# Performance work log

Measured on AMD Instinct MI355X. Metric: run time of the kernel, lower is better.

Reference implementation:

```python
import jax, jax.numpy as jnp
import numpy as np

B, S, I, H, O = 4096, 512, 1, 16, 1


def setup_inputs() -> dict:
    key = jax.random.key(0)
    ks = jax.random.split(key, 7)
    bound = 1.0 / np.sqrt(H)
    return {
        "x": jax.random.normal(ks[0], (B, S, I), dtype=jnp.float32),
        "W_ih": jax.random.uniform(ks[1], (H, I), minval=-bound, maxval=bound, dtype=jnp.float32),
        "W_hh": jax.random.uniform(ks[2], (H, H), minval=-bound, maxval=bound, dtype=jnp.float32),
        "b_ih": jax.random.uniform(ks[3], (H,), minval=-bound, maxval=bound, dtype=jnp.float32),
        "b_hh": jax.random.uniform(ks[4], (H,), minval=-bound, maxval=bound, dtype=jnp.float32),
        "W_fc": jax.random.uniform(ks[5], (O, H), minval=-bound, maxval=bound, dtype=jnp.float32),
        "b_fc": jax.random.uniform(ks[6], (O,), minval=-bound, maxval=bound, dtype=jnp.float32),
    }


def reference(x, W_ih, W_hh, b_ih, b_hh, W_fc, b_fc):
    # Vanilla RNN (tanh): h_t = tanh(x_t W_ih^T + b_ih + h_{t-1} W_hh^T + b_hh)
    # Precompute input projections for all timesteps in one GEMM: [B,S,H]
    x_proj = jnp.einsum('bsi,hi->bsh', x, W_ih) + b_ih + b_hh

    def step(h, xp_t):  # h: [B,H], xp_t: [B,H]
        h_new = jnp.tanh(xp_t + h @ W_hh.T)
        return h_new, None

    h0 = jnp.zeros((x.shape[0], W_hh.shape[0]), dtype=x.dtype)
    h_last, _ = jax.lax.scan(step, h0, jnp.swapaxes(x_proj, 0, 1))  # scan over S
    # out[:, -1, :] -> final linear
    return h_last @ W_fc.T + b_fc
```

## Files before the change

kernel.cpp:

```cpp
#include <hip/hip_runtime.h>


#define S2LE 2.8853900817779268f

typedef float float4_ __attribute__((ext_vector_type(4)));

#define ROTI(v, N) __builtin_amdgcn_mov_dpp((v), 0x120 + (N), 0xF, 0xF, 0)
#define ROTF(v, N) __int_as_float(__builtin_amdgcn_mov_dpp(__float_as_int(v), 0x120 + (N), 0xF, 0xF, 0))

__global__ __launch_bounds__(64) void rnn_kernel(
    const float* __restrict__ x,
    const float* __restrict__ W_ih,
    const float* __restrict__ W_hh,
    const float* __restrict__ b_ih,
    const float* __restrict__ b_hh,
    const float* __restrict__ W_fc,
    const float* __restrict__ b_fc,
    float* __restrict__ out)
{
    const int li = (int)(threadIdx.x & 15u);
    const int bs = (int)((threadIdx.x >> 4) & 1u);
    const int q  = (int)((threadIdx.x >> 5) & 1u);
    const int b  = (int)(blockIdx.x * 2u + bs);

    const float* __restrict__ row = W_hh + li * 16;

    float sw = 0.0f;
#pragma unroll
    for (int j = 0; j < 16; ++j) sw += row[j];

    const float wsc = -2.0f * S2LE;

    const int rq = (li + 8 * q) & 15;
    float w0 = wsc * row[rq];
    float w1 = wsc * row[ROTI(rq, 1)];
    float w2 = wsc * row[ROTI(rq, 2)];
    float w3 = wsc * row[ROTI(rq, 3)];
    float w4 = wsc * row[ROTI(rq, 4)];
    float w5 = wsc * row[ROTI(rq, 5)];
    float w6 = wsc * row[ROTI(rq, 6)];
    float w7 = wsc * row[ROTI(rq, 7)];

    const float wih  = W_ih[li] * S2LE * 0.5f;
    const float bias = (b_ih[li] + b_hh[li] + sw) * S2LE * 0.5f;
    const float wfc  = q ? 0.0f : W_fc[li];
    const float bfc  = b_fc[0];

    const float4_* __restrict__ xv = (const float4_*)(x + (size_t)b * 512);

    float g = 0.5f;

#define STEP(XP) do { \
    float a0 = (XP), a1; \
    asm volatile( \
        "s_nop 1\n\t" \
        "v_fmac_f32 %0, %2, %3\n\t" \
        "v_mul_f32_dpp %1, %2, %7  row_ror:4 row_mask:0xf bank_mask:0xf\n\t" \
        "v_fmac_f32_dpp %0, %2, %4 row_ror:1 row_mask:0xf bank_mask:0xf\n\t" \
        "v_fmac_f32_dpp %1, %2, %8 row_ror:5 row_mask:0xf bank_mask:0xf\n\t" \
        "v_fmac_f32_dpp %0, %2, %5 row_ror:2 row_mask:0xf bank_mask:0xf\n\t" \
        "v_fmac_f32_dpp %1, %2, %9 row_ror:6 row_mask:0xf bank_mask:0xf\n\t" \
        "v_fmac_f32_dpp %0, %2, %6 row_ror:3 row_mask:0xf bank_mask:0xf\n\t" \
        "v_fmac_f32_dpp %1, %2, %10 row_ror:7 row_mask:0xf bank_mask:0xf\n\t" \
        "v_add_f32 %0, %0, %1\n\t"                     \
        "v_mov_b32 %1, %0\n\t"                         \
        "s_nop 1\n\t" \
        "v_permlane32_swap_b32 %1, %0\n\t"             \
        "v_add_f32 %0, %0, %1\n\t"                     \
        "s_nop 1\n\t" \
        "v_mov_b32_dpp %0, %0 row_ror:8 row_mask:0xc bank_mask:0xf\n\t" \
        : "+v"(a0), "=&v"(a1) \
        : "v"(g), \
          "v"(w0), "v"(w1), "v"(w2), "v"(w3), \
          "v"(w4), "v"(w5), "v"(w6), "v"(w7)); \
    float e_ = __builtin_amdgcn_exp2f(a0); \
    g = __builtin_amdgcn_rcpf(e_ + 1.0f); \
} while (0)

#define BLOCK(BUF) do { \
    _Pragma("unroll") \
    for (int j = 0; j < 4; ++j) { \
        STEP(fmaf((BUF)[j][0], wih, bias)); \
        STEP(fmaf((BUF)[j][1], wih, bias)); \
        STEP(fmaf((BUF)[j][2], wih, bias)); \
        STEP(fmaf((BUF)[j][3], wih, bias)); \
    } \
} while (0)

    float4_ bufA[4], bufB[4];
#pragma unroll
    for (int j = 0; j < 4; ++j) bufA[j] = xv[j];

#pragma unroll 1
    for (int i = 0; i < 32; i += 2) {
#pragma unroll
        for (int j = 0; j < 4; ++j) bufB[j] = xv[(4 * (i + 1) + j) & 127];
        BLOCK(bufA);
#pragma unroll
        for (int j = 0; j < 4; ++j) bufA[j] = xv[(4 * (i + 2) + j) & 127];
        BLOCK(bufB);
    }
#undef BLOCK
#undef STEP

    float p = fmaf(-2.0f * wfc, g, wfc);
    p += ROTF(p, 8);
    p += ROTF(p, 4);
    p += ROTF(p, 2);
    p += ROTF(p, 1);
    if ((threadIdx.x & 47u) == 0) out[b] = p + bfc;
}

extern "C" void kernel_launch(void* const* d_in, const int* in_sizes, int n_in,
                              void* d_out, int out_size, void* d_ws, size_t ws_size,
                              hipStream_t stream) {
    const float* x    = (const float*)d_in[0];
    const float* W_ih = (const float*)d_in[1];
    const float* W_hh = (const float*)d_in[2];
    const float* b_ih = (const float*)d_in[3];
    const float* b_hh = (const float*)d_in[4];
    const float* W_fc = (const float*)d_in[5];
    const float* b_fc = (const float*)d_in[6];
    float* out = (float*)d_out;

    rnn_kernel<<<2048, 64, 0, stream>>>(x, W_ih, W_hh, b_ih, b_hh, W_fc, b_fc, out);
}
```

Baseline: 106.4 us.

## Compute recurrent matvec with MFMA f16 hi/lo split, sixteen batches per wave

Replaces the DPP-rotation matvec with two chained v_mfma_f32_16x16x16_f16 ops per timestep. W_hh is split into fp16 high and low parts to keep accuracy, and the hidden state is carried in fp16 as the B operand. Each wave now processes 16 batch rows instead of 2, so the grid shrinks from 2048 to 256 blocks. The aim is to amortise the serial recurrence across more batches per instruction. The cost is fewer waves per CU to hide latency, MFMA latency sitting on the critical path, and rounding the hidden state to fp16.

```diff
diff --git a/kernel.cpp b/kernel.cpp
--- a/kernel.cpp
+++ b/kernel.cpp
@@ -3,10 +3,28 @@
 
 #define S2LE 2.8853900817779268f
 
-typedef float float4_ __attribute__((ext_vector_type(4)));
+typedef float    float4_ __attribute__((ext_vector_type(4)));
+typedef _Float16 half4_  __attribute__((ext_vector_type(4)));
 
-#define ROTI(v, N) __builtin_amdgcn_mov_dpp((v), 0x120 + (N), 0xF, 0xF, 0)
-#define ROTF(v, N) __int_as_float(__builtin_amdgcn_mov_dpp(__float_as_int(v), 0x120 + (N), 0xF, 0xF, 0))
+#if defined(__has_builtin)
+#if __has_builtin(__builtin_amdgcn_mfma_f32_16x16x16f16)
+#define HAVE_MFMA_BUILTIN 1
+#endif
+#endif
+
+#ifdef HAVE_MFMA_BUILTIN
+#define MFMA16(A, B, C) __builtin_amdgcn_mfma_f32_16x16x16f16((A), (B), (C), 0, 0, 0)
+#else
+static __device__ __forceinline__ float4_ mfma16_asm(half4_ a, half4_ b, float4_ c) {
+    asm volatile("s_nop 1\n\t"
+                 "v_mfma_f32_16x16x16_f16 %0, %1, %2, %0\n\t"
+                 "s_nop 7\n\t"
+                 "s_nop 7"
+                 : "+v"(c) : "v"(a), "v"(b));
+    return c;
+}
+#define MFMA16(A, B, C) mfma16_asm((A), (B), (C))
+#endif
 
 __global__ __launch_bounds__(64) void rnn_kernel(
     const float* __restrict__ x,
@@ -18,72 +36,69 @@
     const float* __restrict__ b_fc,
     float* __restrict__ out)
 {
-    const int li = (int)(threadIdx.x & 15u);
-    const int bs = (int)((threadIdx.x >> 4) & 1u);
-    const int q  = (int)((threadIdx.x >> 5) & 1u);
-    const int b  = (int)(blockIdx.x * 2u + bs);
-
-    const float* __restrict__ row = W_hh + li * 16;
-
-    float sw = 0.0f;
-#pragma unroll
-    for (int j = 0; j < 16; ++j) sw += row[j];
+    const int l   = (int)threadIdx.x;
+    const int col = l & 15;
+    const int qr  = l >> 4;
+    const int i4  = qr * 4;
+    const int b   = (int)(blockIdx.x * 16u + (unsigned)col);
 
     const float wsc = -2.0f * S2LE;
 
-    const int rq = (li + 8 * q) & 15;
-    float w0 = wsc * row[rq];
-    float w1 = wsc * row[ROTI(rq, 1)];
-    float w2 = wsc * row[ROTI(rq, 2)];
-    float w3 = wsc * row[ROTI(rq, 3)];
-    float w4 = wsc * row[ROTI(rq, 4)];
-    float w5 = wsc * row[ROTI(rq, 5)];
-    float w6 = wsc * row[ROTI(rq, 6)];
-    float w7 = wsc * row[ROTI(rq, 7)];
+    half4_ a_hi, a_lo;
+#pragma unroll
+    for (int r = 0; r < 4; ++r) {
+        float u = wsc * W_hh[col * 16 + i4 + r];
+        _Float16 hi = (_Float16)u;
+        a_hi[r] = hi;
+        a_lo[r] = (_Float16)(u - (float)hi);
+    }
 
-    const float wih  = W_ih[li] * S2LE * 0.5f;
-    const float bias = (b_ih[li] + b_hh[li] + sw) * S2LE * 0.5f;
-    const float wfc  = q ? 0.0f : W_fc[li];
-    const float bfc  = b_fc[0];
+    float wihS[4], biasS[4], wfcr[4];
+#pragma unroll
+    for (int r = 0; r < 4; ++r) {
+        const int ri = i4 + r;
+        float rs = 0.0f;
+#pragma unroll
+        for (int k = 0; k < 16; ++k) rs += W_hh[ri * 16 + k];
+        wihS[r]  = W_ih[ri] * S2LE;
+        biasS[r] = (rs + b_ih[ri] + b_hh[ri]) * S2LE;
+        wfcr[r]  = W_fc[ri];
+    }
+    float cfc = b_fc[0];
+#pragma unroll
+    for (int k = 0; k < 16; ++k) cfc += W_fc[k];
 
     const float4_* __restrict__ xv = (const float4_*)(x + (size_t)b * 512);
 
-    float g = 0.5f;
+    half4_ gB = {(_Float16)0.5f, (_Float16)0.5f, (_Float16)0.5f, (_Float16)0.5f};
+    float4_ gf = {0.5f, 0.5f, 0.5f, 0.5f};
 
-#define STEP(XP) do { \
-    float a0 = (XP), a1; \
-    asm volatile( \
-        "s_nop 1\n\t" \
-        "v_fmac_f32 %0, %2, %3\n\t" \
-        "v_mul_f32_dpp %1, %2, %7  row_ror:4 row_mask:0xf bank_mask:0xf\n\t" \
-        "v_fmac_f32_dpp %0, %2, %4 row_ror:1 row_mask:0xf bank_mask:0xf\n\t" \
-        "v_fmac_f32_dpp %1, %2, %8 row_ror:5 row_mask:0xf bank_mask:0xf\n\t" \
-        "v_fmac_f32_dpp %0, %2, %5 row_ror:2 row_mask:0xf bank_mask:0xf\n\t" \
-        "v_fmac_f32_dpp %1, %2, %9 row_ror:6 row_mask:0xf bank_mask:0xf\n\t" \
-        "v_fmac_f32_dpp %0, %2, %6 row_ror:3 row_mask:0xf bank_mask:0xf\n\t" \
-        "v_fmac_f32_dpp %1, %2, %10 row_ror:7 row_mask:0xf bank_mask:0xf\n\t" \
-        "v_add_f32 %0, %0, %1\n\t"                     \
-        "v_mov_b32 %1, %0\n\t"                         \
-        "s_nop 1\n\t" \
-        "v_permlane32_swap_b32 %1, %0\n\t"             \
-        "v_add_f32 %0, %0, %1\n\t"                     \
-        "s_nop 1\n\t" \
-        "v_mov_b32_dpp %0, %0 row_ror:8 row_mask:0xc bank_mask:0xf\n\t" \
-        : "+v"(a0), "=&v"(a1) \
-        : "v"(g), \
-          "v"(w0), "v"(w1), "v"(w2), "v"(w3), \
-          "v"(w4), "v"(w5), "v"(w6), "v"(w7)); \
-    float e_ = __builtin_amdgcn_exp2f(a0); \
-    g = __builtin_amdgcn_rcpf(e_ + 1.0f); \
+#define STEP(XT) do { \
+    float xt_ = (XT); \
+    float4_ c; \
+    c[0] = fmaf(xt_, wihS[0], biasS[0]); \
+    c[1] = fmaf(xt_, wihS[1], biasS[1]); \
+    c[2] = fmaf(xt_, wihS[2], biasS[2]); \
+    c[3] = fmaf(xt_, wihS[3], biasS[3]); \
+    c = MFMA16(a_lo, gB, c); \
+    c = MFMA16(a_hi, gB, c); \
+    gf[0] = __builtin_amdgcn_rcpf(__builtin_amdgcn_exp2f(c[0]) + 1.0f); \
+    gf[1] = __builtin_amdgcn_rcpf(__builtin_amdgcn_exp2f(c[1]) + 1.0f); \
+    gf[2] = __builtin_amdgcn_rcpf(__builtin_amdgcn_exp2f(c[2]) + 1.0f); \
+    gf[3] = __builtin_amdgcn_rcpf(__builtin_amdgcn_exp2f(c[3]) + 1.0f); \
+    gB[0] = (_Float16)gf[0]; \
+    gB[1] = (_Float16)gf[1]; \
+    gB[2] = (_Float16)gf[2]; \
+    gB[3] = (_Float16)gf[3]; \
 } while (0)
 
 #define BLOCK(BUF) do { \
     _Pragma("unroll") \
     for (int j = 0; j < 4; ++j) { \
-        STEP(fmaf((BUF)[j][0], wih, bias)); \
-        STEP(fmaf((BUF)[j][1], wih, bias)); \
-        STEP(fmaf((BUF)[j][2], wih, bias)); \
-        STEP(fmaf((BUF)[j][3], wih, bias)); \
+        STEP((BUF)[j][0]); \
+        STEP((BUF)[j][1]); \
+        STEP((BUF)[j][2]); \
+        STEP((BUF)[j][3]); \
     } \
 } while (0)
 
@@ -103,12 +118,10 @@
 #undef BLOCK
 #undef STEP
 
-    float p = fmaf(-2.0f * wfc, g, wfc);
-    p += ROTF(p, 8);
-    p += ROTF(p, 4);
-    p += ROTF(p, 2);
-    p += ROTF(p, 1);
-    if ((threadIdx.x & 47u) == 0) out[b] = p + bfc;
+    float p = gf[0] * wfcr[0] + gf[1] * wfcr[1] + gf[2] * wfcr[2] + gf[3] * wfcr[3];
+    p += __shfl_xor(p, 16, 64);
+    p += __shfl_xor(p, 32, 64);
+    if (qr == 0) out[b] = fmaf(-2.0f, p, cfc);
 }
 
 extern "C" void kernel_launch(void* const* d_in, const int* in_sizes, int n_in,
@@ -123,5 +136,5 @@
     const float* b_fc = (const float*)d_in[6];
     float* out = (float*)d_out;
 
-    rnn_kernel<<<2048, 64, 0, stream>>>(x, W_ih, W_hh, b_ih, b_hh, W_fc, b_fc, out);
+    rnn_kernel<<<256, 64, 0, stream>>>(x, W_ih, W_hh, b_ih, b_hh, W_fc, b_fc, out);
 }
```

Result: slower. 116.9 us (+9.8%).
